# Performance work log

Measured on AMD Instinct MI355X. Metric: run time of the kernel, lower is better.

Reference implementation:

```python
import jax, jax.numpy as jnp
import numpy as np

B, T, D, S = 4, 8192, 512, 16

def setup_inputs() -> dict:
    key = jax.random.key(0)
    k1, k2, k3, k4, k5 = jax.random.split(key, 5)
    x = jax.random.normal(k1, (B, T, D), dtype=jnp.float32)
    # splat parameters as in __init__: centers ~ 0.02*randn, log_scales = 0
    centers = jax.random.normal(k2, (S, D), dtype=jnp.float32) * 0.02
    log_scales = jnp.zeros((S,), dtype=jnp.float32)
    # xavier-uniform linear weights (gain = 1/(1+layer_idx*0.1) = 1.0 for layer 0)
    limit = float(np.sqrt(6.0 / (D + D)))
    Wv = jax.random.uniform(k3, (D, D), minval=-limit, maxval=limit, dtype=jnp.float32)
    Wo = jax.random.uniform(k4, (D, D), minval=-limit, maxval=limit, dtype=jnp.float32)
    return {"x": x, "centers": centers, "log_scales": log_scales, "Wv": Wv, "Wo": Wo}

def reference(x, centers, log_scales, Wv, Wo):
    # scales clamped as in EnhancedAdaptiveSplat.get_scale
    scales = jnp.clip(jnp.exp(log_scales), 0.1, 2.0)           # [S]
    v = jnp.einsum('btd,ed->bte', x, Wv)                       # value projection [B,T,D]
    # squared distance token<->splat via expansion (no [B,T,S,D] intermediate)
    x2 = jnp.sum(x * x, axis=-1, keepdims=True)                # [B,T,1]
    c2 = jnp.sum(centers * centers, axis=-1)                   # [S]
    xc = jnp.einsum('btd,sd->bts', x, centers)                 # [B,T,S]
    d2 = x2 + c2 - 2.0 * xc                                    # [B,T,S]
    logits = -0.5 * d2 / (scales * scales)                     # gaussian kernel log-weights
    attn = jax.nn.softmax(logits, axis=-1)                     # normalize over splats [B,T,S]
    # tokens -> splats aggregation, then splats -> tokens distribution
    splat_states = jnp.einsum('bts,btd->bsd', attn, v)         # [B,S,D]
    out = jnp.einsum('bts,bsd->btd', attn, splat_states)       # [B,T,D]
    return jnp.einsum('btd,ed->bte', out, Wo)                  # output projection
```

## Files before the change

kernel.cpp:

```cpp
#include <hip/hip_runtime.h>
#include <hip/hip_bf16.h>
#include <math.h>

#define B_ 4
#define T_ 8192
#define D_ 512
#define S_ 16

__device__ __forceinline__ float reduce_scatter16(float vals[S_], int lane) {
  {
    const int bit = (lane >> 5) & 1;
#pragma unroll
    for (int i = 0; i < 8; ++i) {
      float send = bit ? vals[i] : vals[i + 8];
      float keep = bit ? vals[i + 8] : vals[i];
      vals[i] = keep + __shfl_xor(send, 32, 64);
    }
  }
  {
    const int bit = (lane >> 4) & 1;
#pragma unroll
    for (int i = 0; i < 4; ++i) {
      float send = bit ? vals[i] : vals[i + 4];
      float keep = bit ? vals[i + 4] : vals[i];
      vals[i] = keep + __shfl_xor(send, 16, 64);
    }
  }
  {
    const int bit = (lane >> 3) & 1;
#pragma unroll
    for (int i = 0; i < 2; ++i) {
      float send = bit ? vals[i] : vals[i + 2];
      float keep = bit ? vals[i + 2] : vals[i];
      vals[i] = keep + __shfl_xor(send, 8, 64);
    }
  }
  {
    const int bit = (lane >> 2) & 1;
    float send = bit ? vals[0] : vals[1];
    float keep = bit ? vals[1] : vals[0];
    float v = keep + __shfl_xor(send, 4, 64);
    v += __shfl_xor(v, 2, 64);
    v += __shfl_xor(v, 1, 64);
    return v;
  }
}

__device__ __forceinline__ float dot4(float4 a, float4 b) {
  return a.x * b.x + a.y * b.y + a.z * b.z + a.w * b.w;
}

__global__ __launch_bounds__(256, 2) void attn_k(const float* __restrict__ x,
                                                 const float* __restrict__ centers,
                                                 const float* __restrict__ log_scales,
                                                 float* __restrict__ attn,
                                                 float* __restrict__ ts) {
  if (blockIdx.x < 64) {
    *(float2*)(ts + blockIdx.x * 512 + threadIdx.x * 2) = make_float2(0.f, 0.f);
  }

  const int lane = threadIdx.x & 63;
  const int wid = (blockIdx.x << 2) + (threadIdx.x >> 6);
  const int nw = gridDim.x << 2;
  const int myS = (lane >> 2) & 15;

  float4 c_reg[S_][2];
#pragma unroll
  for (int s = 0; s < S_; ++s)
#pragma unroll
    for (int j = 0; j < 2; ++j)
      c_reg[s][j] = *(const float4*)(centers + s * D_ + (j << 8) + (lane << 2));

  float c2;
  {
    float vals[S_];
#pragma unroll
    for (int s = 0; s < S_; ++s)
      vals[s] = dot4(c_reg[s][0], c_reg[s][0]) + dot4(c_reg[s][1], c_reg[s][1]);
    c2 = reduce_scatter16(vals, lane);
  }
  const float sc = fminf(fmaxf(__expf(log_scales[myS]), 0.1f), 2.0f);
  const float inv2 = 0.5f / (sc * sc);

  const int npairs = (B_ * T_) / 2;
  for (int tp = wid; tp < npairs; tp += nw) {
    const int t0 = tp << 1;
    const float* xr = x + (size_t)t0 * D_;
    float4 a0 = *(const float4*)(xr + (lane << 2));
    float4 a1 = *(const float4*)(xr + 256 + (lane << 2));
    float4 b0 = *(const float4*)(xr + 512 + (lane << 2));
    float4 b1 = *(const float4*)(xr + 768 + (lane << 2));

    float x2a = dot4(a0, a0) + dot4(a1, a1);
    float x2b = dot4(b0, b0) + dot4(b1, b1);

    float va[S_], vb[S_];
#pragma unroll
    for (int s = 0; s < S_; ++s) {
      va[s] = x2a - 2.f * (dot4(a0, c_reg[s][0]) + dot4(a1, c_reg[s][1]));
      vb[s] = x2b - 2.f * (dot4(b0, c_reg[s][0]) + dot4(b1, c_reg[s][1]));
    }

    float ra = reduce_scatter16(va, lane);
    float rb = reduce_scatter16(vb, lane);
    float la = -(ra + c2) * inv2;
    float lb = -(rb + c2) * inv2;

    float ma = la, mb = lb;
    ma = fmaxf(ma, __shfl_xor(ma, 4, 64));  mb = fmaxf(mb, __shfl_xor(mb, 4, 64));
    ma = fmaxf(ma, __shfl_xor(ma, 8, 64));  mb = fmaxf(mb, __shfl_xor(mb, 8, 64));
    ma = fmaxf(ma, __shfl_xor(ma, 16, 64)); mb = fmaxf(mb, __shfl_xor(mb, 16, 64));
    ma = fmaxf(ma, __shfl_xor(ma, 32, 64)); mb = fmaxf(mb, __shfl_xor(mb, 32, 64));
    float ea = __expf(la - ma), eb = __expf(lb - mb);
    float sa = ea, sb = eb;
    sa += __shfl_xor(sa, 4, 64);  sb += __shfl_xor(sb, 4, 64);
    sa += __shfl_xor(sa, 8, 64);  sb += __shfl_xor(sb, 8, 64);
    sa += __shfl_xor(sa, 16, 64); sb += __shfl_xor(sb, 16, 64);
    sa += __shfl_xor(sa, 32, 64); sb += __shfl_xor(sb, 32, 64);
    if ((lane & 3) == 0) {
      attn[(size_t)t0 * S_ + myS] = ea / sa;
      attn[(size_t)(t0 + 1) * S_ + myS] = eb / sb;
    }
  }
}

#define K2_TOK 128
__global__ __launch_bounds__(512) void ts_k(const float* __restrict__ x,
                                            const float* __restrict__ attn,
                                            float* __restrict__ ts) {
  const int chunks = T_ / K2_TOK;
  const int b = blockIdx.x / chunks;
  const int t0 = (blockIdx.x % chunks) * K2_TOK;
  const int d = threadIdx.x;

  float acc[S_];
#pragma unroll
  for (int s = 0; s < S_; ++s) acc[s] = 0.f;

  const float* xb = x + ((size_t)b * T_ + t0) * D_ + d;
  const float4* ab = (const float4*)(attn + ((size_t)b * T_ + t0) * S_);

#pragma unroll 16
  for (int t = 0; t < K2_TOK; ++t) {
    float xv = xb[(size_t)t * D_];
    float4 a0 = ab[t * 4 + 0], a1 = ab[t * 4 + 1];
    float4 a2 = ab[t * 4 + 2], a3 = ab[t * 4 + 3];
    acc[0]  += a0.x * xv; acc[1]  += a0.y * xv; acc[2]  += a0.z * xv; acc[3]  += a0.w * xv;
    acc[4]  += a1.x * xv; acc[5]  += a1.y * xv; acc[6]  += a1.z * xv; acc[7]  += a1.w * xv;
    acc[8]  += a2.x * xv; acc[9]  += a2.y * xv; acc[10] += a2.z * xv; acc[11] += a2.w * xv;
    acc[12] += a3.x * xv; acc[13] += a3.y * xv; acc[14] += a3.z * xv; acc[15] += a3.w * xv;
  }

  float* tb = ts + (size_t)b * S_ * D_ + d;
#pragma unroll
  for (int s = 0; s < S_; ++s) atomicAdd(tb + s * D_, acc[s]);
}

__global__ __launch_bounds__(256) void proj_k(const float* __restrict__ in,
                                              const float* __restrict__ W,
                                              float* __restrict__ out) {
  __shared__ float red[4][64];
  const int r = blockIdx.x >> 3;
  const int eb = blockIdx.x & 7;
  const int el = threadIdx.x & 63;
  const int kc = threadIdx.x >> 6;
  const int e = (eb << 6) + el;

  const float4* w4 = (const float4*)(W + (size_t)e * D_ + kc * 128);
  const float4* i4 = (const float4*)(in + (size_t)r * D_ + kc * 128);
  float acc = 0.f;
#pragma unroll
  for (int k = 0; k < 32; ++k) acc += dot4(w4[k], i4[k]);

  red[kc][el] = acc;
  __syncthreads();
  if (kc == 0)
    out[(size_t)r * D_ + e] = red[0][el] + red[1][el] + red[2][el] + red[3][el];
}

#define K4_TOK 64
__global__ __launch_bounds__(256) void out_k(const float* __restrict__ attn,
                                             const float* __restrict__ ss_o,
                                             float* __restrict__ out) {
  const int chunks = T_ / K4_TOK;
  const int b = blockIdx.x / chunks;
  const int t0 = (blockIdx.x % chunks) * K4_TOK;
  const int w = threadIdx.x >> 6;
  const int lane = threadIdx.x & 63;
  const int e0 = (w << 7) + (lane << 1);

  float2 ssf[S_];
  const float* sb = ss_o + (size_t)b * S_ * D_;
#pragma unroll
  for (int s = 0; s < S_; ++s) ssf[s] = *(const float2*)(sb + s * D_ + e0);

  const float4* ab = (const float4*)(attn + ((size_t)b * T_ + t0) * S_);
  float* ob = out + ((size_t)b * T_ + t0) * D_ + e0;

#pragma unroll 4
  for (int t = 0; t < K4_TOK; ++t) {
    float4 a0 = ab[t * 4 + 0], a1 = ab[t * 4 + 1];
    float4 a2 = ab[t * 4 + 2], a3 = ab[t * 4 + 3];
    float av[S_] = {a0.x, a0.y, a0.z, a0.w, a1.x, a1.y, a1.z, a1.w,
                    a2.x, a2.y, a2.z, a2.w, a3.x, a3.y, a3.z, a3.w};
    float2 acc = make_float2(0.f, 0.f);
#pragma unroll
    for (int s = 0; s < S_; ++s) {
      acc.x += av[s] * ssf[s].x;
      acc.y += av[s] * ssf[s].y;
    }
    *(float2*)(ob + (size_t)t * D_) = acc;
  }
}

extern "C" void kernel_launch(void* const* d_in, const int* in_sizes, int n_in,
                              void* d_out, int out_size, void* d_ws, size_t ws_size,
                              hipStream_t stream) {
  const float* x          = (const float*)d_in[0];
  const float* centers    = (const float*)d_in[1];
  const float* log_scales = (const float*)d_in[2];
  const float* Wv         = (const float*)d_in[3];
  const float* Wo         = (const float*)d_in[4];
  float* out = (float*)d_out;

  float* attn = (float*)d_ws;
  float* ts   = attn + (size_t)B_ * T_ * S_;
  float* tmp  = ts + (size_t)B_ * S_ * D_;
  float* ss_o = tmp + (size_t)B_ * S_ * D_;

  attn_k<<<2048, 256, 0, stream>>>(x, centers, log_scales, attn, ts);
  ts_k<<<B_ * (T_ / K2_TOK), 512, 0, stream>>>(x, attn, ts);
  proj_k<<<512, 256, 0, stream>>>(ts, Wv, tmp);
  proj_k<<<512, 256, 0, stream>>>(tmp, Wo, ss_o);
  out_k<<<B_ * (T_ / K4_TOK), 256, 0, stream>>>(attn, ss_o, out);
}
```

Before: 194.0 us.

## Fuse splat attention and token-to-splat aggregation into one kernel

Merges the attention kernel and the token-to-splat reduction kernel so each wave reuses its register-held x rows to accumulate attn-weighted sums, avoiding a second full read of x and a round trip through the attn buffer. Each wave now owns a contiguous block of 32 tokens, software-prefetches the next token pair, and flushes 16x512 partial sums with atomics at the end. The zeroing of ts moves to a memset. The grid shrinks to 256 blocks at occupancy 1 with a large register footprint (centers plus 128 accumulator floats), which risks low latency hiding and heavy atomic traffic (1024 waves each adding 8K values).

```diff
diff --git a/kernel.cpp b/kernel.cpp
--- a/kernel.cpp
+++ b/kernel.cpp
@@ -50,18 +50,19 @@
   return a.x * b.x + a.y * b.y + a.z * b.z + a.w * b.w;
 }
 
-__global__ __launch_bounds__(256, 2) void attn_k(const float* __restrict__ x,
-                                                 const float* __restrict__ centers,
-                                                 const float* __restrict__ log_scales,
-                                                 float* __restrict__ attn,
-                                                 float* __restrict__ ts) {
-  if (blockIdx.x < 64) {
-    *(float2*)(ts + blockIdx.x * 512 + threadIdx.x * 2) = make_float2(0.f, 0.f);
-  }
-
+__device__ __forceinline__ void fma4(float4& d, float a, float4 v) {
+  d.x += a * v.x; d.y += a * v.y; d.z += a * v.z; d.w += a * v.w;
+}
+
+__global__ __launch_bounds__(256, 1) void attn_ts_k(const float* __restrict__ x,
+                                                    const float* __restrict__ centers,
+                                                    const float* __restrict__ log_scales,
+                                                    float* __restrict__ attn,
+                                                    float* __restrict__ ts) {
   const int lane = threadIdx.x & 63;
   const int wid = (blockIdx.x << 2) + (threadIdx.x >> 6);
-  const int nw = gridDim.x << 2;
+  const int b = wid >> 8;
+  const int t0 = (wid & 255) * (T_ / 256);
   const int myS = (lane >> 2) & 15;
 
   float4 c_reg[S_][2];
@@ -82,14 +83,31 @@
   const float sc = fminf(fmaxf(__expf(log_scales[myS]), 0.1f), 2.0f);
   const float inv2 = 0.5f / (sc * sc);
 
-  const int npairs = (B_ * T_) / 2;
-  for (int tp = wid; tp < npairs; tp += nw) {
-    const int t0 = tp << 1;
-    const float* xr = x + (size_t)t0 * D_;
-    float4 a0 = *(const float4*)(xr + (lane << 2));
-    float4 a1 = *(const float4*)(xr + 256 + (lane << 2));
-    float4 b0 = *(const float4*)(xr + 512 + (lane << 2));
-    float4 b1 = *(const float4*)(xr + 768 + (lane << 2));
+  float4 tsa[S_][2];
+#pragma unroll
+  for (int s = 0; s < S_; ++s) {
+    tsa[s][0] = make_float4(0.f, 0.f, 0.f, 0.f);
+    tsa[s][1] = make_float4(0.f, 0.f, 0.f, 0.f);
+  }
+
+  const float* xr = x + ((size_t)b * T_ + t0) * D_;
+  float* ar = attn + ((size_t)b * T_ + t0) * S_;
+
+  float4 na0 = *(const float4*)(xr + (lane << 2));
+  float4 na1 = *(const float4*)(xr + 256 + (lane << 2));
+  float4 nb0 = *(const float4*)(xr + 512 + (lane << 2));
+  float4 nb1 = *(const float4*)(xr + 768 + (lane << 2));
+
+#pragma unroll 1
+  for (int tt = 0; tt < 32; tt += 2) {
+    float4 a0 = na0, a1 = na1, b0 = nb0, b1 = nb1;
+    if (tt + 2 < 32) {
+      const float* nx = xr + (size_t)(tt + 2) * D_;
+      na0 = *(const float4*)(nx + (lane << 2));
+      na1 = *(const float4*)(nx + 256 + (lane << 2));
+      nb0 = *(const float4*)(nx + 512 + (lane << 2));
+      nb1 = *(const float4*)(nx + 768 + (lane << 2));
+    }
 
     float x2a = dot4(a0, a0) + dot4(a1, a1);
     float x2b = dot4(b0, b0) + dot4(b1, b1);
@@ -117,43 +135,34 @@
     sa += __shfl_xor(sa, 8, 64);  sb += __shfl_xor(sb, 8, 64);
     sa += __shfl_xor(sa, 16, 64); sb += __shfl_xor(sb, 16, 64);
     sa += __shfl_xor(sa, 32, 64); sb += __shfl_xor(sb, 32, 64);
+    float aa = ea / sa, ab2 = eb / sb;
+
     if ((lane & 3) == 0) {
-      attn[(size_t)t0 * S_ + myS] = ea / sa;
-      attn[(size_t)(t0 + 1) * S_ + myS] = eb / sb;
-    }
-  }
-}
-
-#define K2_TOK 128
-__global__ __launch_bounds__(512) void ts_k(const float* __restrict__ x,
-                                            const float* __restrict__ attn,
-                                            float* __restrict__ ts) {
-  const int chunks = T_ / K2_TOK;
-  const int b = blockIdx.x / chunks;
-  const int t0 = (blockIdx.x % chunks) * K2_TOK;
-  const int d = threadIdx.x;
-
-  float acc[S_];
-#pragma unroll
-  for (int s = 0; s < S_; ++s) acc[s] = 0.f;
-
-  const float* xb = x + ((size_t)b * T_ + t0) * D_ + d;
-  const float4* ab = (const float4*)(attn + ((size_t)b * T_ + t0) * S_);
-
-#pragma unroll 16
-  for (int t = 0; t < K2_TOK; ++t) {
-    float xv = xb[(size_t)t * D_];
-    float4 a0 = ab[t * 4 + 0], a1 = ab[t * 4 + 1];
-    float4 a2 = ab[t * 4 + 2], a3 = ab[t * 4 + 3];
-    acc[0]  += a0.x * xv; acc[1]  += a0.y * xv; acc[2]  += a0.z * xv; acc[3]  += a0.w * xv;
-    acc[4]  += a1.x * xv; acc[5]  += a1.y * xv; acc[6]  += a1.z * xv; acc[7]  += a1.w * xv;
-    acc[8]  += a2.x * xv; acc[9]  += a2.y * xv; acc[10] += a2.z * xv; acc[11] += a2.w * xv;
-    acc[12] += a3.x * xv; acc[13] += a3.y * xv; acc[14] += a3.z * xv; acc[15] += a3.w * xv;
-  }
-
-  float* tb = ts + (size_t)b * S_ * D_ + d;
-#pragma unroll
-  for (int s = 0; s < S_; ++s) atomicAdd(tb + s * D_, acc[s]);
+      ar[(size_t)tt * S_ + myS] = aa;
+      ar[(size_t)(tt + 1) * S_ + myS] = ab2;
+    }
+
+#pragma unroll
+    for (int s = 0; s < S_; ++s) {
+      float as = __shfl(aa, s << 2, 64);
+      float bs = __shfl(ab2, s << 2, 64);
+      fma4(tsa[s][0], as, a0); fma4(tsa[s][1], as, a1);
+      fma4(tsa[s][0], bs, b0); fma4(tsa[s][1], bs, b1);
+    }
+  }
+
+  float* tb = ts + (size_t)b * S_ * D_;
+#pragma unroll
+  for (int s = 0; s < S_; ++s) {
+#pragma unroll
+    for (int j = 0; j < 2; ++j) {
+      float* p = tb + s * D_ + (j << 8) + (lane << 2);
+      atomicAdd(p + 0, tsa[s][j].x);
+      atomicAdd(p + 1, tsa[s][j].y);
+      atomicAdd(p + 2, tsa[s][j].z);
+      atomicAdd(p + 3, tsa[s][j].w);
+    }
+  }
 }
 
 __global__ __launch_bounds__(256) void proj_k(const float* __restrict__ in,
@@ -228,8 +237,9 @@
   float* tmp  = ts + (size_t)B_ * S_ * D_;
   float* ss_o = tmp + (size_t)B_ * S_ * D_;
 
-  attn_k<<<2048, 256, 0, stream>>>(x, centers, log_scales, attn, ts);
-  ts_k<<<B_ * (T_ / K2_TOK), 512, 0, stream>>>(x, attn, ts);
+  hipMemsetAsync(ts, 0, (size_t)B_ * S_ * D_ * sizeof(float), stream);
+
+  attn_ts_k<<<256, 256, 0, stream>>>(x, centers, log_scales, attn, ts);
   proj_k<<<512, 256, 0, stream>>>(ts, Wv, tmp);
   proj_k<<<512, 256, 0, stream>>>(tmp, Wo, ss_o);
   out_k<<<B_ * (T_ / K4_TOK), 256, 0, stream>>>(attn, ss_o, out);
```

After: 413.2 us. 2.13x slower.
